# Kernel tuning notes

Measured on AMD Instinct MI355X. Metric: run time of the kernel, lower is better.

The kernel has to match this reference:

```python
import jax, jax.numpy as jnp
import numpy as np

HIDDEN = 2048
INTER = 4096
NUM_EXPERTS = 8
TOP_K = 4
BATCH, SEQ = 2, 2048
TOKENS = BATCH * SEQ


def setup_inputs() -> dict:
    key = jax.random.key(0)
    k_x, k_rw, k_tw, k_te, k_gu, k_dn = jax.random.split(key, 6)
    x = jax.random.normal(k_x, (BATCH, SEQ, HIDDEN), dtype=jnp.float32)
    # full router weights (passed through but unused by this patched forward)
    weights = jax.random.uniform(k_rw, (TOKENS, NUM_EXPERTS), dtype=jnp.float32)
    tw = jax.random.uniform(k_tw, (TOKENS, TOP_K), dtype=jnp.float32)
    top_weights = tw / jnp.sum(tw, axis=-1, keepdims=True)  # softmax-like, renormalize=False downstream
    top_experts = jax.random.randint(k_te, (TOKENS, TOP_K), 0, NUM_EXPERTS, dtype=jnp.int64)
    scale_gu = 1.0 / np.sqrt(HIDDEN)
    scale_dn = 1.0 / np.sqrt(INTER)
    gate_up_weights = jax.random.normal(k_gu, (NUM_EXPERTS, 2 * INTER, HIDDEN), dtype=jnp.float32) * scale_gu
    down_weights = jax.random.normal(k_dn, (NUM_EXPERTS, HIDDEN, INTER), dtype=jnp.float32) * scale_dn
    return {
        'x': x,
        'weights': weights,
        'top_weights': top_weights,
        'top_experts': top_experts,
        'gate_up_weights': gate_up_weights,
        'down_weights': down_weights,
    }


def _fused_moe(xf, gate_up_weights, down_weights, top_weights, top_experts):
    """xf: [T, D]. Dense per-expert loop (scan over experts), masked combine.

    Matches fused_moe(renormalize=False): out[t] = sum_k top_weights[t,k] * expert_{top_experts[t,k]}(x[t])
    expert(x) = (silu(x @ Wg^T) * (x @ Wu^T)) @ Wd^T with [Wg; Wu] = gate_up.
    """
    E = gate_up_weights.shape[0]

    def step(out, inp):
        w_gu, w_d, e = inp
        # per-token combine coefficient for this expert (0 if not routed)
        coef = jnp.sum(jnp.where(top_experts == e, top_weights, 0.0), axis=-1)  # [T]
        h = xf @ w_gu.T                       # [T, 2*INTER]
        gate, up = jnp.split(h, 2, axis=-1)
        act = jax.nn.silu(gate) * up          # [T, INTER]
        o = act @ w_d.T                       # [T, D]
        return out + coef[:, None] * o, None

    out, _ = jax.lax.scan(step, jnp.zeros_like(xf),
                          (gate_up_weights, down_weights, jnp.arange(E, dtype=jnp.int64)))
    return out


def reference(x, weights, top_weights, top_experts, gate_up_weights, down_weights):
    B, S, D = x.shape
    xf = x.reshape(-1, D)  # flatten(0, 1)
    out = _fused_moe(xf, gate_up_weights, down_weights, top_weights, top_experts)
    return out.reshape(B, S, D)  # unflatten(0, (-1, q_len))
```

## Files before the change

### kernel.cpp

```cpp
#include <hip/hip_runtime.h>
#include <stdint.h>

#define T_TOKENS 4096
#define D_HID    2048
#define D_INT    4096
#define N_EXP    8
#define TOPK     4
#define NFLAT    (T_TOKENS*TOPK)
#define BM       128
#define MAXPAD   (NFLAT + N_EXP*BM)
#define MTILES   (MAXPAD/BM)

#define OFF_XB   0ull
#define OFF_ACT  16777216ull
#define OFF_PTOK 159383552ull
#define OFF_PWT  159453184ull
#define OFF_CNT  159522816ull
#define OFF_TOFF 159523072ull
#define OFF_SEG  159531264ull

typedef float f32x4  __attribute__((ext_vector_type(4)));
typedef short bf16x8 __attribute__((ext_vector_type(8)));

__device__ __forceinline__ unsigned short f2bf(float f) {
    unsigned int u = __float_as_uint(f);
    u += 0x7fffu + ((u >> 16) & 1u);
    return (unsigned short)(u >> 16);
}

__device__ __forceinline__ void gload_lds16(const void* g, void* l) {
    __builtin_amdgcn_global_load_lds((const __attribute__((address_space(1))) void*)g,
                                     (__attribute__((address_space(3))) void*)l,
                                     16, 0, 0);
}

__global__ void k_prep(const float* __restrict__ x, unsigned short* __restrict__ xb,
                       float* __restrict__ out) {
    int i = blockIdx.x * 256 + threadIdx.x;
    float4 v = ((const float4*)x)[i];
    ushort4 h;
    h.x = f2bf(v.x); h.y = f2bf(v.y); h.z = f2bf(v.z); h.w = f2bf(v.w);
    ((ushort4*)xb)[i] = h;
    ((float4*)out)[i] = make_float4(0.f, 0.f, 0.f, 0.f);
}

__global__ void k_count(const int* __restrict__ te, int* __restrict__ counts,
                        int* __restrict__ toff) {
    int e = blockIdx.x, t = threadIdx.x;
    int cnt = 0;
    int base = t * 64;
    for (int i = 0; i < 64; i++) cnt += (te[base + i] == e);
    __shared__ int s[256];
    s[t] = cnt; __syncthreads();
    int incl = cnt;
    for (int off = 1; off < 256; off <<= 1) {
        int tmp = (t >= off) ? s[t - off] : 0;
        __syncthreads();
        incl += tmp; s[t] = incl;
        __syncthreads();
    }
    toff[e * 256 + t] = incl - cnt;
    if (t == 255) counts[e] = incl;
}

__global__ void k_fill(const int* __restrict__ te, const float* __restrict__ tw,
                       const int* __restrict__ counts, const int* __restrict__ toff,
                       int* __restrict__ ptok, float* __restrict__ pwt, int* __restrict__ seg) {
    int e = blockIdx.x, t = threadIdx.x;
    int segs[9]; int a = 0;
    #pragma unroll
    for (int j = 0; j < 8; j++) { segs[j] = a; a += (counts[j] + BM - 1) & ~(BM - 1); }
    segs[8] = a;
    if (e == 0 && t == 0) { for (int j = 0; j < 9; j++) seg[j] = segs[j]; }
    int base = segs[e] + toff[e * 256 + t];
    int rank = 0;
    for (int i = t * 64; i < (t + 1) * 64; i++) {
        if (te[i] == e) { ptok[base + rank] = i >> 2; pwt[base + rank] = tw[i]; rank++; }
    }
    int cnt = counts[e], pc = (cnt + BM - 1) & ~(BM - 1);
    for (int i = cnt + t; i < pc; i += 256) { ptok[segs[e] + i] = -1; pwt[segs[e] + i] = 0.f; }
}

__launch_bounds__(256, 2)
__global__ void k_gemm1(const unsigned short* __restrict__ xb, const float* __restrict__ wgu,
                        const int* __restrict__ ptok, const int* __restrict__ seg,
                        unsigned short* __restrict__ act) {
    __shared__ char lds[32768];
    char* lA = lds; char* lB = lds + 16384;
    int nb = blockIdx.x, mb = blockIdx.y;
    if (mb * BM >= seg[8]) return;
    int e = 0;
    #pragma unroll
    for (int j = 1; j < 8; j++) if (seg[j] <= mb * BM) e = j;
    int tid = threadIdx.x, w = tid >> 6, l = tid & 63;

    const char* asrc[4]; char* adst[4];
    #pragma unroll
    for (int i = 0; i < 4; i++) {
        int row = w * 32 + i * 8 + (l >> 3);
        int tok = ptok[mb * BM + row]; if (tok < 0) tok = 0;
        int csrc = (l & 7) ^ (row & 7);
        asrc[i] = (const char*)(xb + (size_t)tok * D_HID + csrc * 8);
        adst[i] = lA + (w * 32 + i * 8) * 128;
    }
    const float* bsrc[8]; int bdst[8];
    #pragma unroll
    for (int j = 0; j < 8; j++) {
        int flat = j * 1024 + tid * 4;
        int r = flat >> 6, c = flat & 63;
        size_t grow = (r < 64) ? (size_t)(nb * 64 + r) : (size_t)(D_INT + nb * 64 + (r - 64));
        bsrc[j] = wgu + (size_t)e * 2 * D_INT * D_HID + grow * D_HID + c;
        bdst[j] = r * 128 + ((c * 2) ^ ((r & 7) << 4));
    }

    f32x4 acc[2][8];
    #pragma unroll
    for (int m = 0; m < 2; m++)
        #pragma unroll
        for (int n = 0; n < 8; n++) acc[m][n] = (f32x4){0.f, 0.f, 0.f, 0.f};

    for (int k0 = 0; k0 < D_HID; k0 += 64) {
        #pragma unroll
        for (int i = 0; i < 4; i++) gload_lds16(asrc[i] + (size_t)k0 * 2, adst[i]);
        #pragma unroll
        for (int j = 0; j < 8; j++) {
            float4 v = *(const float4*)(bsrc[j] + k0);
            ushort4 h;
            h.x = f2bf(v.x); h.y = f2bf(v.y); h.z = f2bf(v.z); h.w = f2bf(v.w);
            *(ushort4*)(lB + bdst[j]) = h;
        }
        __syncthreads();
        #pragma unroll
        for (int kk = 0; kk < 2; kk++) {
            bf16x8 a[2], b[8];
            #pragma unroll
            for (int m = 0; m < 2; m++) {
                int row = w * 32 + m * 16 + (l & 15);
                int kb = kk * 64 + (l >> 4) * 16;
                a[m] = *(const bf16x8*)(lA + row * 128 + (kb ^ ((row & 7) << 4)));
            }
            #pragma unroll
            for (int n = 0; n < 8; n++) {
                int row = n * 16 + (l & 15);
                int kb = kk * 64 + (l >> 4) * 16;
                b[n] = *(const bf16x8*)(lB + row * 128 + (kb ^ ((row & 7) << 4)));
            }
            #pragma unroll
            for (int m = 0; m < 2; m++)
                #pragma unroll
                for (int n = 0; n < 8; n++)
                    acc[m][n] = __builtin_amdgcn_mfma_f32_16x16x32_bf16(a[m], b[n], acc[m][n], 0, 0, 0);
        }
        __syncthreads();
    }
    #pragma unroll
    for (int m = 0; m < 2; m++)
        #pragma unroll
        for (int n = 0; n < 4; n++) {
            f32x4 g = acc[m][n], u = acc[m][n + 4];
            #pragma unroll
            for (int r = 0; r < 4; r++) {
                float gv = g[r], uv = u[r];
                float av = gv / (1.f + __expf(-gv)) * uv;
                int row = w * 32 + m * 16 + (l >> 4) * 4 + r;
                int col = nb * 64 + n * 16 + (l & 15);
                act[(size_t)(mb * BM + row) * D_INT + col] = f2bf(av);
            }
        }
}

__launch_bounds__(256, 2)
__global__ void k_gemm2(const unsigned short* __restrict__ act, const float* __restrict__ wd,
                        const int* __restrict__ ptok, const float* __restrict__ pwt,
                        const int* __restrict__ seg, float* __restrict__ out) {
    __shared__ char lds[32768];
    char* lA = lds; char* lB = lds + 16384;
    int nb = blockIdx.x, mb = blockIdx.y;
    if (mb * BM >= seg[8]) return;
    int e = 0;
    #pragma unroll
    for (int j = 1; j < 8; j++) if (seg[j] <= mb * BM) e = j;
    int tid = threadIdx.x, w = tid >> 6, l = tid & 63;

    const char* asrc[4]; char* adst[4];
    #pragma unroll
    for (int i = 0; i < 4; i++) {
        int row = w * 32 + i * 8 + (l >> 3);
        int csrc = (l & 7) ^ (row & 7);
        asrc[i] = (const char*)(act + (size_t)(mb * BM + row) * D_INT + csrc * 8);
        adst[i] = lA + (w * 32 + i * 8) * 128;
    }
    const float* bsrc[8]; int bdst[8];
    #pragma unroll
    for (int j = 0; j < 8; j++) {
        int flat = j * 1024 + tid * 4;
        int r = flat >> 6, c = flat & 63;
        bsrc[j] = wd + (size_t)e * D_HID * D_INT + (size_t)(nb * BM + r) * D_INT + c;
        bdst[j] = r * 128 + ((c * 2) ^ ((r & 7) << 4));
    }

    f32x4 acc[2][8];
    #pragma unroll
    for (int m = 0; m < 2; m++)
        #pragma unroll
        for (int n = 0; n < 8; n++) acc[m][n] = (f32x4){0.f, 0.f, 0.f, 0.f};

    for (int k0 = 0; k0 < D_INT; k0 += 64) {
        #pragma unroll
        for (int i = 0; i < 4; i++) gload_lds16(asrc[i] + (size_t)k0 * 2, adst[i]);
        #pragma unroll
        for (int j = 0; j < 8; j++) {
            float4 v = *(const float4*)(bsrc[j] + k0);
            ushort4 h;
            h.x = f2bf(v.x); h.y = f2bf(v.y); h.z = f2bf(v.z); h.w = f2bf(v.w);
            *(ushort4*)(lB + bdst[j]) = h;
        }
        __syncthreads();
        #pragma unroll
        for (int kk = 0; kk < 2; kk++) {
            bf16x8 a[2], b[8];
            #pragma unroll
            for (int m = 0; m < 2; m++) {
                int row = w * 32 + m * 16 + (l & 15);
                int kb = kk * 64 + (l >> 4) * 16;
                a[m] = *(const bf16x8*)(lA + row * 128 + (kb ^ ((row & 7) << 4)));
            }
            #pragma unroll
            for (int n = 0; n < 8; n++) {
                int row = n * 16 + (l & 15);
                int kb = kk * 64 + (l >> 4) * 16;
                b[n] = *(const bf16x8*)(lB + row * 128 + (kb ^ ((row & 7) << 4)));
            }
            #pragma unroll
            for (int m = 0; m < 2; m++)
                #pragma unroll
                for (int n = 0; n < 8; n++)
                    acc[m][n] = __builtin_amdgcn_mfma_f32_16x16x32_bf16(a[m], b[n], acc[m][n], 0, 0, 0);
        }
        __syncthreads();
    }
    #pragma unroll
    for (int m = 0; m < 2; m++) {
        #pragma unroll
        for (int r = 0; r < 4; r++) {
            int row = w * 32 + m * 16 + (l >> 4) * 4 + r;
            int p = mb * BM + row;
            int tok = ptok[p];
            float wt = pwt[p];
            if (tok >= 0) {
                #pragma unroll
                for (int n = 0; n < 8; n++) {
                    int col = nb * BM + n * 16 + (l & 15);
                    unsafeAtomicAdd(&out[(size_t)tok * D_HID + col], wt * acc[m][n][r]);
                }
            }
        }
    }
}

extern "C" void kernel_launch(void* const* d_in, const int* in_sizes, int n_in,
                              void* d_out, int out_size, void* d_ws, size_t ws_size,
                              hipStream_t stream) {
    const float* x   = (const float*)d_in[0];
    const float* tw  = (const float*)d_in[2];
    const int*   te  = (const int*)d_in[3];
    const float* wgu = (const float*)d_in[4];
    const float* wd  = (const float*)d_in[5];
    float* out = (float*)d_out;
    char*  ws  = (char*)d_ws;

    unsigned short* xb  = (unsigned short*)(ws + OFF_XB);
    unsigned short* act = (unsigned short*)(ws + OFF_ACT);
    int*   ptok   = (int*)(ws + OFF_PTOK);
    float* pwt    = (float*)(ws + OFF_PWT);
    int*   counts = (int*)(ws + OFF_CNT);
    int*   toff   = (int*)(ws + OFF_TOFF);
    int*   seg    = (int*)(ws + OFF_SEG);

    k_prep<<<8192, 256, 0, stream>>>(x, xb, out);
    k_count<<<N_EXP, 256, 0, stream>>>(te, counts, toff);
    k_fill<<<N_EXP, 256, 0, stream>>>(te, tw, counts, toff, ptok, pwt, seg);
    k_gemm1<<<dim3(D_INT / 64, MTILES), 256, 0, stream>>>(xb, wgu, ptok, seg, act);
    k_gemm2<<<dim3(D_HID / BM, MTILES), 256, 0, stream>>>(act, wd, ptok, pwt, seg, out);
}
```

Measured before the change: 1.378 ms.

## Rewrite MoE GEMMs with bf16 pre-cast weights, 256-row tiles and 4-stage LDS pipeline

Weights are now cast from fp32 to bf16 in separate kernels before each GEMM, so the GEMMs stream bf16 operands straight into LDS with global_load_lds instead of converting inside the inner loop. Both GEMMs move to 512-thread blocks with 256-row tiles, a 4-deep LDS ring buffer with explicit waitcnt, barriers and setprio scheduling, and XCD-aware block remapping. The down-projection also splits K in two halves accumulated through atomics. The extra cast passes add full-weight read/write traffic each call in exchange for denser MFMA pipelines and better operand reuse.

```diff
diff --git a/kernel.cpp b/kernel.cpp
--- a/kernel.cpp
+++ b/kernel.cpp
@@ -7,17 +7,18 @@
 #define N_EXP    8
 #define TOPK     4
 #define NFLAT    (T_TOKENS*TOPK)
-#define BM       128
-#define MAXPAD   (NFLAT + N_EXP*BM)
-#define MTILES   (MAXPAD/BM)
-
-#define OFF_XB   0ull
-#define OFF_ACT  16777216ull
-#define OFF_PTOK 159383552ull
-#define OFF_PWT  159453184ull
-#define OFF_CNT  159522816ull
-#define OFF_TOFF 159523072ull
-#define OFF_SEG  159531264ull
+#define BMT      256
+#define MAXPAD   (NFLAT + N_EXP*BMT)
+#define MT2      (MAXPAD/BMT)
+
+#define OFF_PTOK 0ull
+#define OFF_PWT  73728ull
+#define OFF_CNT  147456ull
+#define OFF_TOFF 147712ull
+#define OFF_SEG  155904ull
+#define OFF_XB   262144ull
+#define OFF_ACT  17039360ull
+#define OFF_W    168034304ull
 
 typedef float f32x4  __attribute__((ext_vector_type(4)));
 typedef short bf16x8 __attribute__((ext_vector_type(8)));
@@ -32,6 +33,12 @@
     __builtin_amdgcn_global_load_lds((const __attribute__((address_space(1))) void*)g,
                                      (__attribute__((address_space(3))) void*)l,
                                      16, 0, 0);
+}
+
+__device__ __forceinline__ int xcd_logical(int hw, int nwg) {
+    int q = nwg >> 3, r = nwg & 7;
+    int xc = hw & 7, sl = hw >> 3;
+    return (xc < r ? xc * (q + 1) : r * (q + 1) + (xc - r) * q) + sl;
 }
 
 __global__ void k_prep(const float* __restrict__ x, unsigned short* __restrict__ xb,
@@ -42,6 +49,14 @@
     h.x = f2bf(v.x); h.y = f2bf(v.y); h.z = f2bf(v.z); h.w = f2bf(v.w);
     ((ushort4*)xb)[i] = h;
     ((float4*)out)[i] = make_float4(0.f, 0.f, 0.f, 0.f);
+}
+
+__global__ void k_cast(const float* __restrict__ src, unsigned short* __restrict__ dst) {
+    size_t i = (size_t)blockIdx.x * 256 + threadIdx.x;
+    float4 v = ((const float4*)src)[i];
+    ushort4 h;
+    h.x = f2bf(v.x); h.y = f2bf(v.y); h.z = f2bf(v.z); h.w = f2bf(v.w);
+    ((ushort4*)dst)[i] = h;
 }
 
 __global__ void k_count(const int* __restrict__ te, int* __restrict__ counts,
@@ -69,7 +84,7 @@
     int e = blockIdx.x, t = threadIdx.x;
     int segs[9]; int a = 0;
     #pragma unroll
-    for (int j = 0; j < 8; j++) { segs[j] = a; a += (counts[j] + BM - 1) & ~(BM - 1); }
+    for (int j = 0; j < 8; j++) { segs[j] = a; a += (counts[j] + BMT - 1) & ~(BMT - 1); }
     segs[8] = a;
     if (e == 0 && t == 0) { for (int j = 0; j < 9; j++) seg[j] = segs[j]; }
     int base = segs[e] + toff[e * 256 + t];
@@ -77,180 +92,166 @@
     for (int i = t * 64; i < (t + 1) * 64; i++) {
         if (te[i] == e) { ptok[base + rank] = i >> 2; pwt[base + rank] = tw[i]; rank++; }
     }
-    int cnt = counts[e], pc = (cnt + BM - 1) & ~(BM - 1);
+    int cnt = counts[e], pc = (cnt + BMT - 1) & ~(BMT - 1);
     for (int i = cnt + t; i < pc; i += 256) { ptok[segs[e] + i] = -1; pwt[segs[e] + i] = 0.f; }
 }
 
-__launch_bounds__(256, 2)
-__global__ void k_gemm1(const unsigned short* __restrict__ xb, const float* __restrict__ wgu,
-                        const int* __restrict__ ptok, const int* __restrict__ seg,
-                        unsigned short* __restrict__ act) {
-    __shared__ char lds[32768];
-    char* lA = lds; char* lB = lds + 16384;
-    int nb = blockIdx.x, mb = blockIdx.y;
-    if (mb * BM >= seg[8]) return;
+
+#define KSTEP(VMS) \
+  asm volatile("s_waitcnt vmcnt(" VMS ")" ::: "memory"); \
+  __builtin_amdgcn_s_barrier(); \
+  __builtin_amdgcn_sched_barrier(0); \
+  { \
+    const char* pT = ldsc + (cb << 15); \
+    bf16x8 af[8], bf[4]; \
+    _Pragma("unroll") for (int m_ = 0; m_ < 8; ++m_) \
+        af[m_] = *(const bf16x8*)(pT + a_off + m_ * 1024); \
+    _Pragma("unroll") for (int n_ = 0; n_ < 4; ++n_) \
+        bf[n_] = *(const bf16x8*)(pT + b_off + n_ * 1024); \
+    asm volatile("s_waitcnt lgkmcnt(0)" ::: "memory"); \
+    __builtin_amdgcn_sched_barrier(0); \
+    __builtin_amdgcn_s_barrier(); \
+    __builtin_amdgcn_s_setprio(1); \
+    _Pragma("unroll") for (int m_ = 0; m_ < 8; ++m_) \
+      _Pragma("unroll") for (int n_ = 0; n_ < 4; ++n_) \
+        acc[m_][n_] = __builtin_amdgcn_mfma_f32_16x16x32_bf16(af[m_], bf[n_], acc[m_][n_], 0, 0, 0); \
+    __builtin_amdgcn_s_setprio(0); \
+    cb = (cb + 1) & 3; \
+  }
+
+__global__ void __launch_bounds__(512, 2)
+k_g1(const unsigned short* __restrict__ xb, const unsigned short* __restrict__ wgu_b,
+     const int* __restrict__ ptok, const int* __restrict__ seg,
+     unsigned short* __restrict__ act) {
+    extern __shared__ char smem[];
+    char* ldsw = smem; const char* ldsc = smem;
+    int logical = xcd_logical(blockIdx.x, 2304);
+    int nb = logical / MT2, mb = logical % MT2;
+    if (mb * BMT >= seg[8]) return;
     int e = 0;
     #pragma unroll
-    for (int j = 1; j < 8; j++) if (seg[j] <= mb * BM) e = j;
+    for (int j = 1; j < 8; ++j) if (seg[j] <= mb * BMT) e = j;
     int tid = threadIdx.x, w = tid >> 6, l = tid & 63;
-
-    const char* asrc[4]; char* adst[4];
-    #pragma unroll
-    for (int i = 0; i < 4; i++) {
-        int row = w * 32 + i * 8 + (l >> 3);
-        int tok = ptok[mb * BM + row]; if (tok < 0) tok = 0;
-        int csrc = (l & 7) ^ (row & 7);
-        asrc[i] = (const char*)(xb + (size_t)tok * D_HID + csrc * 8);
-        adst[i] = lA + (w * 32 + i * 8) * 128;
-    }
-    const float* bsrc[8]; int bdst[8];
-    #pragma unroll
-    for (int j = 0; j < 8; j++) {
-        int flat = j * 1024 + tid * 4;
-        int r = flat >> 6, c = flat & 63;
-        size_t grow = (r < 64) ? (size_t)(nb * 64 + r) : (size_t)(D_INT + nb * 64 + (r - 64));
-        bsrc[j] = wgu + (size_t)e * 2 * D_INT * D_HID + grow * D_HID + c;
-        bdst[j] = r * 128 + ((c * 2) ^ ((r & 7) << 4));
-    }
-
-    f32x4 acc[2][8];
-    #pragma unroll
-    for (int m = 0; m < 2; m++)
-        #pragma unroll
-        for (int n = 0; n < 8; n++) acc[m][n] = (f32x4){0.f, 0.f, 0.f, 0.f};
-
-    for (int k0 = 0; k0 < D_HID; k0 += 64) {
-        #pragma unroll
-        for (int i = 0; i < 4; i++) gload_lds16(asrc[i] + (size_t)k0 * 2, adst[i]);
-        #pragma unroll
-        for (int j = 0; j < 8; j++) {
-            float4 v = *(const float4*)(bsrc[j] + k0);
-            ushort4 h;
-            h.x = f2bf(v.x); h.y = f2bf(v.y); h.z = f2bf(v.z); h.w = f2bf(v.w);
-            *(ushort4*)(lB + bdst[j]) = h;
-        }
-        __syncthreads();
-        #pragma unroll
-        for (int kk = 0; kk < 2; kk++) {
-            bf16x8 a[2], b[8];
+    int wr = w >> 2, wc = w & 3;
+
+    int g = (l & 3) ^ ((l >> 3) & 3);
+    int r0 = w * 16 + (l >> 2), r1 = 128 + r0;
+    int t0 = ptok[mb * BMT + r0]; if (t0 < 0) t0 = 0;
+    int t1 = ptok[mb * BMT + r1]; if (t1 < 0) t1 = 0;
+    const char* pa0 = (const char*)xb + (size_t)t0 * 4096 + g * 16;
+    const char* pa1 = (const char*)xb + (size_t)t1 * 4096 + g * 16;
+    int wcr0 = r0 >> 6, j0 = r0 & 63;
+    int wcr1 = r1 >> 6, j1 = r1 & 63;
+    int gr0 = (j0 < 32) ? (nb * 128 + wcr0 * 32 + j0) : (D_INT + nb * 128 + wcr0 * 32 + j0 - 32);
+    int gr1 = (j1 < 32) ? (nb * 128 + wcr1 * 32 + j1) : (D_INT + nb * 128 + wcr1 * 32 + j1 - 32);
+    const char* wbase = (const char*)wgu_b + (size_t)e * 8192 * 4096;
+    const char* pb0 = wbase + (size_t)gr0 * 4096 + g * 16;
+    const char* pb1 = wbase + (size_t)gr1 * 4096 + g * 16;
+    int dA0 = w * 1024, dA1 = 8192 + w * 1024;
+    int dB0 = 16384 + w * 1024, dB1 = 24576 + w * 1024;
+    int sb = 0;
+    auto STAGE = [&]() {
+        char* d = ldsw + (sb << 15);
+        gload_lds16(pa0, d + dA0); gload_lds16(pa1, d + dA1);
+        gload_lds16(pb0, d + dB0); gload_lds16(pb1, d + dB1);
+        pa0 += 64; pa1 += 64; pb0 += 64; pb1 += 64;
+        sb = (sb + 1) & 3;
+    };
+
+    int off_frag = (l & 15) * 64 + ((((l >> 4)) ^ (((l & 15) >> 1) & 3)) << 4);
+    int a_off = wr * 8192 + off_frag;
+    int b_off = 16384 + wc * 4096 + off_frag;
+
+    f32x4 acc[8][4];
+    #pragma unroll
+    for (int m = 0; m < 8; ++m)
+        #pragma unroll
+        for (int n = 0; n < 4; ++n) acc[m][n] = (f32x4){0.f, 0.f, 0.f, 0.f};
+
+    int cb = 0;
+    STAGE(); STAGE(); STAGE();
+    for (int kt = 0; kt < 61; ++kt) { STAGE(); KSTEP("12") }
+    KSTEP("8") KSTEP("4") KSTEP("0")
+
+    int mbase = mb * BMT;
+    #pragma unroll
+    for (int m = 0; m < 8; ++m) {
+        int rowl = wr * 128 + m * 16 + (l >> 4) * 4;
+        #pragma unroll
+        for (int np = 0; np < 2; ++np) {
+            int col = nb * 128 + wc * 32 + np * 16 + (l & 15);
             #pragma unroll
-            for (int m = 0; m < 2; m++) {
-                int row = w * 32 + m * 16 + (l & 15);
-                int kb = kk * 64 + (l >> 4) * 16;
-                a[m] = *(const bf16x8*)(lA + row * 128 + (kb ^ ((row & 7) << 4)));
-            }
-            #pragma unroll
-            for (int n = 0; n < 8; n++) {
-                int row = n * 16 + (l & 15);
-                int kb = kk * 64 + (l >> 4) * 16;
-                b[n] = *(const bf16x8*)(lB + row * 128 + (kb ^ ((row & 7) << 4)));
-            }
-            #pragma unroll
-            for (int m = 0; m < 2; m++)
-                #pragma unroll
-                for (int n = 0; n < 8; n++)
-                    acc[m][n] = __builtin_amdgcn_mfma_f32_16x16x32_bf16(a[m], b[n], acc[m][n], 0, 0, 0);
-        }
-        __syncthreads();
-    }
-    #pragma unroll
-    for (int m = 0; m < 2; m++)
-        #pragma unroll
-        for (int n = 0; n < 4; n++) {
-            f32x4 g = acc[m][n], u = acc[m][n + 4];
-            #pragma unroll
-            for (int r = 0; r < 4; r++) {
-                float gv = g[r], uv = u[r];
+            for (int r = 0; r < 4; ++r) {
+                float gv = acc[m][np][r], uv = acc[m][np + 2][r];
                 float av = gv / (1.f + __expf(-gv)) * uv;
-                int row = w * 32 + m * 16 + (l >> 4) * 4 + r;
-                int col = nb * 64 + n * 16 + (l & 15);
-                act[(size_t)(mb * BM + row) * D_INT + col] = f2bf(av);
+                act[(size_t)(mbase + rowl + r) * D_INT + col] = f2bf(av);
             }
         }
-}
-
-__launch_bounds__(256, 2)
-__global__ void k_gemm2(const unsigned short* __restrict__ act, const float* __restrict__ wd,
-                        const int* __restrict__ ptok, const float* __restrict__ pwt,
-                        const int* __restrict__ seg, float* __restrict__ out) {
-    __shared__ char lds[32768];
-    char* lA = lds; char* lB = lds + 16384;
-    int nb = blockIdx.x, mb = blockIdx.y;
-    if (mb * BM >= seg[8]) return;
+    }
+}
+
+__global__ void __launch_bounds__(512, 2)
+k_g2(const unsigned short* __restrict__ act, const unsigned short* __restrict__ wd_b,
+     const int* __restrict__ ptok, const float* __restrict__ pwt,
+     const int* __restrict__ seg, float* __restrict__ out) {
+    extern __shared__ char smem[];
+    char* ldsw = smem; const char* ldsc = smem;
+    int logical = xcd_logical(blockIdx.x, 1152);
+    int pair = logical / MT2, mb = logical % MT2;
+    int nb = pair >> 1, ks = pair & 1;
+    if (mb * BMT >= seg[8]) return;
     int e = 0;
     #pragma unroll
-    for (int j = 1; j < 8; j++) if (seg[j] <= mb * BM) e = j;
+    for (int j = 1; j < 8; ++j) if (seg[j] <= mb * BMT) e = j;
     int tid = threadIdx.x, w = tid >> 6, l = tid & 63;
-
-    const char* asrc[4]; char* adst[4];
-    #pragma unroll
-    for (int i = 0; i < 4; i++) {
-        int row = w * 32 + i * 8 + (l >> 3);
-        int csrc = (l & 7) ^ (row & 7);
-        asrc[i] = (const char*)(act + (size_t)(mb * BM + row) * D_INT + csrc * 8);
-        adst[i] = lA + (w * 32 + i * 8) * 128;
-    }
-    const float* bsrc[8]; int bdst[8];
-    #pragma unroll
-    for (int j = 0; j < 8; j++) {
-        int flat = j * 1024 + tid * 4;
-        int r = flat >> 6, c = flat & 63;
-        bsrc[j] = wd + (size_t)e * D_HID * D_INT + (size_t)(nb * BM + r) * D_INT + c;
-        bdst[j] = r * 128 + ((c * 2) ^ ((r & 7) << 4));
-    }
-
-    f32x4 acc[2][8];
-    #pragma unroll
-    for (int m = 0; m < 2; m++)
-        #pragma unroll
-        for (int n = 0; n < 8; n++) acc[m][n] = (f32x4){0.f, 0.f, 0.f, 0.f};
-
-    for (int k0 = 0; k0 < D_INT; k0 += 64) {
-        #pragma unroll
-        for (int i = 0; i < 4; i++) gload_lds16(asrc[i] + (size_t)k0 * 2, adst[i]);
-        #pragma unroll
-        for (int j = 0; j < 8; j++) {
-            float4 v = *(const float4*)(bsrc[j] + k0);
-            ushort4 h;
-            h.x = f2bf(v.x); h.y = f2bf(v.y); h.z = f2bf(v.z); h.w = f2bf(v.w);
-            *(ushort4*)(lB + bdst[j]) = h;
-        }
-        __syncthreads();
-        #pragma unroll
-        for (int kk = 0; kk < 2; kk++) {
-            bf16x8 a[2], b[8];
-            #pragma unroll
-            for (int m = 0; m < 2; m++) {
-                int row = w * 32 + m * 16 + (l & 15);
-                int kb = kk * 64 + (l >> 4) * 16;
-                a[m] = *(const bf16x8*)(lA + row * 128 + (kb ^ ((row & 7) << 4)));
-            }
-            #pragma unroll
-            for (int n = 0; n < 8; n++) {
-                int row = n * 16 + (l & 15);
-                int kb = kk * 64 + (l >> 4) * 16;
-                b[n] = *(const bf16x8*)(lB + row * 128 + (kb ^ ((row & 7) << 4)));
-            }
-            #pragma unroll
-            for (int m = 0; m < 2; m++)
-                #pragma unroll
-                for (int n = 0; n < 8; n++)
-                    acc[m][n] = __builtin_amdgcn_mfma_f32_16x16x32_bf16(a[m], b[n], acc[m][n], 0, 0, 0);
-        }
-        __syncthreads();
-    }
-    #pragma unroll
-    for (int m = 0; m < 2; m++) {
-        #pragma unroll
-        for (int r = 0; r < 4; r++) {
-            int row = w * 32 + m * 16 + (l >> 4) * 4 + r;
-            int p = mb * BM + row;
+    int wr = w >> 2, wc = w & 3;
+    int koff = ks * 4096;
+
+    int g = (l & 3) ^ ((l >> 3) & 3);
+    int r0 = w * 16 + (l >> 2), r1 = 128 + r0;
+    const char* pa0 = (const char*)act + (size_t)(mb * BMT + r0) * 8192 + koff + g * 16;
+    const char* pa1 = (const char*)act + (size_t)(mb * BMT + r1) * 8192 + koff + g * 16;
+    const char* wbase = (const char*)wd_b + (size_t)e * D_HID * 8192;
+    const char* pb0 = wbase + (size_t)(nb * 256 + r0) * 8192 + koff + g * 16;
+    const char* pb1 = wbase + (size_t)(nb * 256 + r1) * 8192 + koff + g * 16;
+    int dA0 = w * 1024, dA1 = 8192 + w * 1024;
+    int dB0 = 16384 + w * 1024, dB1 = 24576 + w * 1024;
+    int sb = 0;
+    auto STAGE = [&]() {
+        char* d = ldsw + (sb << 15);
+        gload_lds16(pa0, d + dA0); gload_lds16(pa1, d + dA1);
+        gload_lds16(pb0, d + dB0); gload_lds16(pb1, d + dB1);
+        pa0 += 64; pa1 += 64; pb0 += 64; pb1 += 64;
+        sb = (sb + 1) & 3;
+    };
+
+    int off_frag = (l & 15) * 64 + ((((l >> 4)) ^ (((l & 15) >> 1) & 3)) << 4);
+    int a_off = wr * 8192 + off_frag;
+    int b_off = 16384 + wc * 4096 + off_frag;
+
+    f32x4 acc[8][4];
+    #pragma unroll
+    for (int m = 0; m < 8; ++m)
+        #pragma unroll
+        for (int n = 0; n < 4; ++n) acc[m][n] = (f32x4){0.f, 0.f, 0.f, 0.f};
+
+    int cb = 0;
+    STAGE(); STAGE(); STAGE();
+    for (int kt = 0; kt < 61; ++kt) { STAGE(); KSTEP("12") }
+    KSTEP("8") KSTEP("4") KSTEP("0")
+
+    #pragma unroll
+    for (int m = 0; m < 8; ++m) {
+        int rowl = wr * 128 + m * 16 + (l >> 4) * 4;
+        #pragma unroll
+        for (int r = 0; r < 4; ++r) {
+            int p = mb * BMT + rowl + r;
             int tok = ptok[p];
             float wt = pwt[p];
             if (tok >= 0) {
                 #pragma unroll
-                for (int n = 0; n < 8; n++) {
-                    int col = nb * BM + n * 16 + (l & 15);
+                for (int n = 0; n < 4; ++n) {
+                    int col = nb * 256 + wc * 64 + n * 16 + (l & 15);
                     unsafeAtomicAdd(&out[(size_t)tok * D_HID + col], wt * acc[m][n][r]);
                 }
             }
@@ -269,17 +270,24 @@
     float* out = (float*)d_out;
     char*  ws  = (char*)d_ws;
 
-    unsigned short* xb  = (unsigned short*)(ws + OFF_XB);
-    unsigned short* act = (unsigned short*)(ws + OFF_ACT);
     int*   ptok   = (int*)(ws + OFF_PTOK);
     float* pwt    = (float*)(ws + OFF_PWT);
     int*   counts = (int*)(ws + OFF_CNT);
     int*   toff   = (int*)(ws + OFF_TOFF);
     int*   seg    = (int*)(ws + OFF_SEG);
+    unsigned short* xb  = (unsigned short*)(ws + OFF_XB);
+    unsigned short* act = (unsigned short*)(ws + OFF_ACT);
+    unsigned short* w_b = (unsigned short*)(ws + OFF_W);
+
+    hipFuncSetAttribute((const void*)k_g1, hipFuncAttributeMaxDynamicSharedMemorySize, 131072);
+    hipFuncSetAttribute((const void*)k_g2, hipFuncAttributeMaxDynamicSharedMemorySize, 131072);
 
     k_prep<<<8192, 256, 0, stream>>>(x, xb, out);
     k_count<<<N_EXP, 256, 0, stream>>>(te, counts, toff);
     k_fill<<<N_EXP, 256, 0, stream>>>(te, tw, counts, toff, ptok, pwt, seg);
-    k_gemm1<<<dim3(D_INT / 64, MTILES), 256, 0, stream>>>(xb, wgu, ptok, seg, act);
-    k_gemm2<<<dim3(D_HID / BM, MTILES), 256, 0, stream>>>(act, wd, ptok, pwt, seg, out);
-}
+
+    k_cast<<<131072, 256, 0, stream>>>(wgu, w_b);
+    k_g1<<<2304, 512, 131072, stream>>>(xb, w_b, ptok, seg, act);
+    k_cast<<<65536, 256, 0, stream>>>(wd, w_b);
+    k_g2<<<1152, 512, 131072, stream>>>(act, w_b, ptok, pwt, seg, out);
+}
```

Measured after the change: 1.268 ms. 7.9% less time.
